# Optimization experiments

Measured on AMD Instinct MI355X. Metric: run time of the kernel, lower is better.

The kernel has to match this reference:

```python
import jax, jax.numpy as jnp
import numpy as np

IN_FEATURES = 8192
OUT_FEATURES = 28672


def setup_inputs() -> dict:
    key = jax.random.key(0)
    k1, k2, k3, k4 = jax.random.split(key, 4)
    x = jax.random.normal(k1, (1, IN_FEATURES), dtype=jnp.float32)
    # packed int4 codes: two 4-bit codes per uint8 byte (low nibble = even col, high nibble = odd col)
    qweight = jax.random.randint(k2, (OUT_FEATURES, IN_FEATURES // 2), 0, 256, dtype=jnp.int32).astype(jnp.uint8)
    # per-output-row 16-entry codebook (K-means values), indexed by the 4-bit code
    kmvalues = jax.random.normal(k3, (OUT_FEATURES, 16), dtype=jnp.float32)
    bias = jax.random.normal(k4, (OUT_FEATURES,), dtype=jnp.float32) * 0.01
    return {"x": x, "qweight": qweight, "kmvalues": kmvalues, "bias": bias}


def reference(x, qweight, kmvalues, bias):
    # Unpack two 4-bit codes per byte; matches pack_to_i4: byte = lo | (hi << 4)
    lo = (qweight & 0xF).astype(jnp.int32)   # even columns
    hi = (qweight >> 4).astype(jnp.int32)    # odd columns
    codes = jnp.stack([lo, hi], axis=-1).reshape(qweight.shape[0], -1)  # (O, I)
    # Dequantize via per-row 16-entry lookup table
    W = jnp.take_along_axis(kmvalues, codes, axis=1)  # (O, I) float32
    # Single-token matvec: y = x @ W^T + bias
    y = x @ W.T + bias  # (1, O)
    return y
```

## Files before the change

kernel.cpp:

```cpp
#include <hip/hip_runtime.h>
#include <stdint.h>


typedef _Float16 half2_t __attribute__((ext_vector_type(2)));

#define OUT_F     28672
#define ROW_ELEMS 4096
#define NBLOCKS   1024
#define WPB       4
#define NWAVES    (NBLOCKS * WPB)
#define RPW       (OUT_F / NWAVES)

__device__ __forceinline__ float dot2acc(half2_t a, half2_t b, float c) {
#if __has_builtin(__builtin_amdgcn_fdot2)
    return __builtin_amdgcn_fdot2(a, b, c, false);
#else
    return c + (float)a.x * (float)b.x + (float)a.y * (float)b.y;
#endif
}

__global__ __launch_bounds__(256) void q4lut_matvec(
    const float* __restrict__ x,
    const int*   __restrict__ qw,
    const float* __restrict__ kmv,
    const float* __restrict__ bias,
    float* __restrict__ out)
{
    __shared__ uint32_t pairlut[WPB][256];

    const int tid   = threadIdx.x;
    const int wave  = tid >> 6;
    const int lane  = tid & 63;
    const int gwave = blockIdx.x * WPB + wave;

    half2_t xp[64];
#pragma unroll
    for (int c = 0; c < 16; ++c) {
        const float4* xs = reinterpret_cast<const float4*>(x + c * 512 + lane * 8);
        float4 v0 = xs[0];
        float4 v1 = xs[1];
        xp[c * 4 + 0] = half2_t{(_Float16)v0.x, (_Float16)v0.y};
        xp[c * 4 + 1] = half2_t{(_Float16)v0.z, (_Float16)v0.w};
        xp[c * 4 + 2] = half2_t{(_Float16)v1.x, (_Float16)v1.y};
        xp[c * 4 + 3] = half2_t{(_Float16)v1.z, (_Float16)v1.w};
    }

    for (int r = 0; r < RPW; ++r) {
        const int row = gwave + NWAVES * r;

        const uint4* qrow =
            reinterpret_cast<const uint4*>(qw + (size_t)row * ROW_ELEMS);
        uint4 cs[16];
#pragma unroll
        for (int c = 0; c < 16; ++c) cs[c] = qrow[c * 64 + lane];

        const float    myv = kmv[row * 16 + (lane & 15)];
        const _Float16 hih = (_Float16)__shfl(myv, lane >> 2, 64);
        uint32_t ent[4];
#pragma unroll
        for (int k = 0; k < 4; ++k) {
            const _Float16 loh = (_Float16)__shfl(myv, ((lane & 3) << 2) + k, 64);
            half2_t p = {loh, hih};
            ent[k] = __builtin_bit_cast(uint32_t, p);
        }
        *reinterpret_cast<uint4*>(&pairlut[wave][lane * 4]) =
            make_uint4(ent[0], ent[1], ent[2], ent[3]);

        __syncthreads();

        float acc = 0.f;
#pragma unroll
        for (int c = 0; c < 16; ++c) {
            const uint32_t dws[4] = {cs[c].x, cs[c].y, cs[c].z, cs[c].w};
#pragma unroll
            for (int k = 0; k < 4; ++k) {
                const uint32_t idx = dws[k] & 0xffu;
                const uint32_t pw  = pairlut[wave][idx];
                acc = dot2acc(xp[c * 4 + k], __builtin_bit_cast(half2_t, pw), acc);
            }
        }

#pragma unroll
        for (int off = 32; off > 0; off >>= 1)
            acc += __shfl_xor(acc, off, 64);
        if (lane == 0) out[row] = acc + bias[row];
    }
}

extern "C" void kernel_launch(void* const* d_in, const int* in_sizes, int n_in,
                              void* d_out, int out_size, void* d_ws, size_t ws_size,
                              hipStream_t stream) {
    const float* x    = (const float*)d_in[0];
    const int*   qw   = (const int*)d_in[1];
    const float* kmv  = (const float*)d_in[2];
    const float* bias = (const float*)d_in[3];
    float*       out  = (float*)d_out;

    hipLaunchKernelGGL(q4lut_matvec, dim3(NBLOCKS), dim3(256), 0, stream,
                       x, qw, kmv, bias, out);
}
```

Measured before the change: 599.1 us.

## Prebuild all per-row LUTs and double-buffer packed weight loads across rows

Builds the pair lookup tables for all rows a wave handles before the main loop and drops the per-row __syncthreads. It also splits each row's weight fetch into two halves and prefetches the next row's half while the current half is being consumed. The aim is to overlap global memory latency with LUT/dot work and remove barrier stalls. The cost is more shared memory (RPW x larger) and more live registers, which may lower occupancy.

```diff
diff --git a/kernel.cpp b/kernel.cpp
--- a/kernel.cpp
+++ b/kernel.cpp
@@ -26,7 +26,7 @@
     const float* __restrict__ bias,
     float* __restrict__ out)
 {
-    __shared__ uint32_t pairlut[WPB][256];
+    __shared__ uint32_t pairlut[WPB][RPW][256];
 
     const int tid   = threadIdx.x;
     const int wave  = tid >> 6;
@@ -45,16 +45,12 @@
         xp[c * 4 + 3] = half2_t{(_Float16)v1.z, (_Float16)v1.w};
     }
 
+    float biasv[RPW];
+#pragma unroll
     for (int r = 0; r < RPW; ++r) {
         const int row = gwave + NWAVES * r;
-
-        const uint4* qrow =
-            reinterpret_cast<const uint4*>(qw + (size_t)row * ROW_ELEMS);
-        uint4 cs[16];
-#pragma unroll
-        for (int c = 0; c < 16; ++c) cs[c] = qrow[c * 64 + lane];
-
-        const float    myv = kmv[row * 16 + (lane & 15)];
+        const float myv = kmv[row * 16 + (lane & 15)];
+        biasv[r] = bias[row];
         const _Float16 hih = (_Float16)__shfl(myv, lane >> 2, 64);
         uint32_t ent[4];
 #pragma unroll
@@ -63,27 +59,63 @@
             half2_t p = {loh, hih};
             ent[k] = __builtin_bit_cast(uint32_t, p);
         }
-        *reinterpret_cast<uint4*>(&pairlut[wave][lane * 4]) =
+        *reinterpret_cast<uint4*>(&pairlut[wave][r][lane * 4]) =
             make_uint4(ent[0], ent[1], ent[2], ent[3]);
+    }
 
-        __syncthreads();
+    uint4 A[8], B[8];
+    {
+        const uint4* q0 =
+            reinterpret_cast<const uint4*>(qw + (size_t)gwave * ROW_ELEMS);
+#pragma unroll
+        for (int c = 0; c < 8; ++c) A[c] = q0[c * 64 + lane];
+#pragma unroll
+        for (int c = 0; c < 8; ++c) B[c] = q0[(c + 8) * 64 + lane];
+    }
+
+#pragma unroll
+    for (int r = 0; r < RPW; ++r) {
+        const int row = gwave + NWAVES * r;
+        const uint4* qn = reinterpret_cast<const uint4*>(
+            qw + (size_t)(row + NWAVES) * ROW_ELEMS);
 
         float acc = 0.f;
+
 #pragma unroll
-        for (int c = 0; c < 16; ++c) {
-            const uint32_t dws[4] = {cs[c].x, cs[c].y, cs[c].z, cs[c].w};
+        for (int c = 0; c < 8; ++c) {
+            const uint32_t dws[4] = {A[c].x, A[c].y, A[c].z, A[c].w};
 #pragma unroll
             for (int k = 0; k < 4; ++k) {
                 const uint32_t idx = dws[k] & 0xffu;
-                const uint32_t pw  = pairlut[wave][idx];
-                acc = dot2acc(xp[c * 4 + k], __builtin_bit_cast(half2_t, pw), acc);
+                acc = dot2acc(xp[c * 4 + k],
+                              __builtin_bit_cast(half2_t, pairlut[wave][r][idx]),
+                              acc);
             }
+        }
+        if (r + 1 < RPW) {
+#pragma unroll
+            for (int c = 0; c < 8; ++c) A[c] = qn[c * 64 + lane];
+        }
+#pragma unroll
+        for (int c = 8; c < 16; ++c) {
+            const uint32_t dws[4] = {B[c - 8].x, B[c - 8].y, B[c - 8].z, B[c - 8].w};
+#pragma unroll
+            for (int k = 0; k < 4; ++k) {
+                const uint32_t idx = dws[k] & 0xffu;
+                acc = dot2acc(xp[c * 4 + k],
+                              __builtin_bit_cast(half2_t, pairlut[wave][r][idx]),
+                              acc);
+            }
+        }
+        if (r + 1 < RPW) {
+#pragma unroll
+            for (int c = 0; c < 8; ++c) B[c] = qn[(c + 8) * 64 + lane];
         }
 
 #pragma unroll
         for (int off = 32; off > 0; off >>= 1)
             acc += __shfl_xor(acc, off, 64);
-        if (lane == 0) out[row] = acc + bias[row];
+        if (lane == 0) out[row] = acc + biasv[r];
     }
 }
 
```

Measured after the change: 601.4 us. About the same (+0.4%).
